# Optimization experiments

Measured on AMD Instinct MI355X. Metric: run time of the kernel, lower is better.

## Reference

```python
import jax, jax.numpy as jnp
import numpy as np

RHO = 0.5
MASK = 1.0
FR0 = 4096  # ifft length along fast-time axis
FR1 = 512   # fft length along slow-time (Doppler) axis
WIN = 8     # sliding-window length of the phase-reference accumulator
EPS_DENOM = 1e-6


def setup_inputs() -> dict:
    key = jax.random.key(0)
    k1, k2 = jax.random.split(key)
    x_real = jax.random.normal(k1, (8, 4096, 256), dtype=jnp.float32)
    x_imag = jax.random.normal(k2, (8, 4096, 256), dtype=jnp.float32)
    return {"x_real": x_real, "x_imag": x_imag}


def _phase_com_doppler(inp):
    # inp: [B, N, M_in] complex; ifft along last axis padded/truncated to FR0
    final = jnp.fft.ifft(inp, n=FR0, axis=2)  # [B, N, M]
    B, N, M = final.shape
    out0 = final[:, 0, :]                      # [B, M]
    # reproduces the torch `if k < 7` branch without control flow.
    buf0 = jnp.zeros((WIN, B, M), final.dtype).at[WIN - 1].set(out0)

    def step(carry, f_k1):
        pref, buf = carry
        s = jnp.sum(jnp.conj(pref) * f_k1, axis=-1, keepdims=True)  # [B,1]
        phase = s / jnp.abs(s)
        o = f_k1 * jnp.conj(phase)                                  # [B,M]
        pref = pref + o - buf[0]
        buf = jnp.concatenate([buf[1:], o[None]], axis=0)
        return (pref, buf), o

    seq = jnp.swapaxes(final, 0, 1)[1:]        # [N-1, B, M]
    _, outs = jax.lax.scan(step, (out0, buf0), seq)
    out = jnp.concatenate([out0[None], outs], axis=0)  # [N, B, M]
    out = jnp.swapaxes(out, 0, 1)              # [B, N, M]
    # fft along pulse axis padded to FR1
    return jnp.fft.fft(out, n=FR1, axis=1)     # [B, FR1, M]


def reference(x_real, x_imag):
    x = jax.lax.complex(x_real, x_imag)        # [B, P, Q] complex64
    denom = MASK + RHO
    denom = EPS_DENOM if denom == 0 else denom
    x2 = x * (1.0 / denom)
    out3 = _phase_com_doppler(jnp.swapaxes(x2, -1, -2))  # [B, FR1, FR0]
    out3 = jnp.swapaxes(out3, -1, -2)          # [B, FR0, FR1]
    # cs_data dict -> tuple ('input', 'nnline_input')
    return (x, out3)
```

## Files before the change

### kernel.cpp

```cpp
#include <hip/hip_runtime.h>
#include <math.h>

#define NF 4096
#define NC 256
#define NJ 512
#define CH 128
#define TWO_PI_F 6.28318530717958647692f

__device__ __forceinline__ float2 cmul(float2 a, float2 b) {
    return make_float2(a.x*b.x - a.y*b.y, a.x*b.y + a.y*b.x);
}

__device__ __forceinline__ void dft4i(float2& x0, float2& x1, float2& x2, float2& x3, float sgn) {
    float2 t0 = make_float2(x0.x + x2.x, x0.y + x2.y);
    float2 t1 = make_float2(x0.x - x2.x, x0.y - x2.y);
    float2 t2 = make_float2(x1.x + x3.x, x1.y + x3.y);
    float2 t3 = make_float2(x1.x - x3.x, x1.y - x3.y);
    float2 it3 = make_float2(-sgn * t3.y, sgn * t3.x);
    x0 = make_float2(t0.x + t2.x, t0.y + t2.y);
    x2 = make_float2(t0.x - t2.x, t0.y - t2.y);
    x1 = make_float2(t1.x + it3.x, t1.y + it3.y);
    x3 = make_float2(t1.x - it3.x, t1.y - it3.y);
}

__device__ __forceinline__ void dft16(float2* u, float sgn) {
    dft4i(u[0], u[4], u[8],  u[12], sgn);
    dft4i(u[1], u[5], u[9],  u[13], sgn);
    dft4i(u[2], u[6], u[10], u[14], sgn);
    dft4i(u[3], u[7], u[11], u[15], sgn);
    const float C1 = 0.9238795325112867f, S1 = 0.3826834323650898f, R2 = 0.7071067811865476f;
    u[5]  = cmul(u[5],  make_float2(C1,  sgn * S1));
    u[6]  = cmul(u[6],  make_float2(R2,  sgn * R2));
    u[7]  = cmul(u[7],  make_float2(S1,  sgn * C1));
    u[9]  = cmul(u[9],  make_float2(R2,  sgn * R2));
    u[10] = cmul(u[10], make_float2(0.f, sgn));
    u[11] = cmul(u[11], make_float2(-R2, sgn * R2));
    u[13] = cmul(u[13], make_float2(S1,  sgn * C1));
    u[14] = cmul(u[14], make_float2(-R2, sgn * R2));
    u[15] = cmul(u[15], make_float2(-C1, -sgn * S1));
    dft4i(u[0],  u[1],  u[2],  u[3],  sgn);
    dft4i(u[4],  u[5],  u[6],  u[7],  sgn);
    dft4i(u[8],  u[9],  u[10], u[11], sgn);
    dft4i(u[12], u[13], u[14], u[15], sgn);
}

__device__ __forceinline__ void dft8(const float2* u, float2* v, float sgn) {
    float2 e0 = u[0], e1 = u[2], e2 = u[4], e3 = u[6];
    float2 o0 = u[1], o1 = u[3], o2 = u[5], o3 = u[7];
    dft4i(e0, e1, e2, e3, sgn);
    dft4i(o0, o1, o2, o3, sgn);
    const float R2 = 0.7071067811865476f;
    float2 w1 = make_float2(R2, sgn * R2);
    float2 w2 = make_float2(0.f, sgn);
    float2 w3 = make_float2(-R2, sgn * R2);
    float2 t1 = cmul(o1, w1), t2 = cmul(o2, w2), t3 = cmul(o3, w3);
    v[0] = make_float2(e0.x + o0.x, e0.y + o0.y);
    v[4] = make_float2(e0.x - o0.x, e0.y - o0.y);
    v[1] = make_float2(e1.x + t1.x, e1.y + t1.y);
    v[5] = make_float2(e1.x - t1.x, e1.y - t1.y);
    v[2] = make_float2(e2.x + t2.x, e2.y + t2.y);
    v[6] = make_float2(e2.x - t2.x, e2.y - t2.y);
    v[3] = make_float2(e3.x + t3.x, e3.y + t3.y);
    v[7] = make_float2(e3.x - t3.x, e3.y - t3.y);
}

__global__ __launch_bounds__(256) void transpose_kernel(const float* __restrict__ xr,
                                                        const float* __restrict__ xi,
                                                        float2* __restrict__ fin,
                                                        int b0, int nbm1, int nbshift) {
    __shared__ float ldr[64][65];
    __shared__ float ldi[64][65];
    int wg = blockIdx.x;
    int bl = wg & nbm1;
    int rest = wg >> nbshift;
    int ft = rest & 63;
    int ct = rest >> 6;
    int f0 = ft << 6, c0 = ct << 6;
    int t = threadIdx.x;
    int cl = t & 63;
    int rq = t >> 6;
    const float scale = 1.0f / (4096.0f * 1.5f);
    int bg = b0 + bl;
    const float* xrb = xr + (size_t)bg * NF * NC;
    const float* xib = xi + (size_t)bg * NF * NC;
#pragma unroll
    for (int q = 0; q < 16; q++) {
        int r = q * 4 + rq;
        size_t idx = (size_t)(f0 + r) * NC + c0 + cl;
        ldr[cl][r] = xrb[idx] * scale;
        ldi[cl][r] = xib[idx] * scale;
    }
    __syncthreads();
    int fl = t & 63;
#pragma unroll
    for (int q = 0; q < 16; q++) {
        int cr = q * 4 + rq;
        fin[((size_t)(bl * NC + c0 + cr)) * NF + f0 + fl] =
            make_float2(ldr[cr][fl], ldi[cr][fl]);
    }
}

#define IPAD(a) ((a) + ((a) >> 4))

template<int P>
__device__ __forceinline__ void pass16(float2* S, int t, float sgn) {
    const int k = t & (P - 1);
    float2 u[16];
#pragma unroll
    for (int r = 0; r < 16; r++) u[r] = S[IPAD(t + 256 * r)];
    __syncthreads();
    if (P > 1) {
        float ab = sgn * (TWO_PI_F / (16.0f * (float)P)) * (float)k;
#pragma unroll
        for (int r = 1; r < 16; r++) {
            float sn, cs; __sincosf(ab * (float)r, &sn, &cs);
            u[r] = cmul(u[r], make_float2(cs, sn));
        }
    }
    dft16(u, sgn);
    const int base = 16 * P * (t / P) + k;
#pragma unroll
    for (int j = 0; j < 16; j++) {
        const int sl = ((j & 3) << 2) | (j >> 2);
        S[IPAD(base + j * P)] = u[sl];
    }
    __syncthreads();
}

__global__ __launch_bounds__(256) void ifft4096_kernel(float2* __restrict__ fin,
                                                       int bmask, int bshift) {
    __shared__ float2 S[4352];
    int wg = blockIdx.x;
    int bl = wg & bmask;
    int c = wg >> bshift;
    int t = threadIdx.x;
    size_t base = ((size_t)(bl * NC + c)) * NF;
    const float4* g4 = (const float4*)(fin + base);
#pragma unroll
    for (int q = 0; q < 8; q++) {
        float4 v = g4[t + 256 * q];
        int f = 2 * (t + 256 * q);
        S[IPAD(f)]     = make_float2(v.x, v.y);
        S[IPAD(f + 1)] = make_float2(v.z, v.w);
    }
    __syncthreads();
    pass16<1>(S, t, 1.0f);
    pass16<16>(S, t, 1.0f);
    pass16<256>(S, t, 1.0f);
    float4* o4 = (float4*)(fin + base);
#pragma unroll
    for (int q = 0; q < 8; q++) {
        int f = 2 * (t + 256 * q);
        float2 a = S[IPAD(f)];
        float2 b = S[IPAD(f + 1)];
        o4[t + 256 * q] = make_float4(a.x, a.y, b.x, b.y);
    }
}

#define GST 142
__global__ __launch_bounds__(256) void gram_kernel(const float2* __restrict__ fin,
                                                   float2* __restrict__ gpart) {
    __shared__ float2 lfc[40 * GST];
    int wg = blockIdx.x;
    int bl = wg >> 8;
    int ks = (wg >> 5) & 7;
    int ch = wg & 31;
    int m0 = ch * CH;
    int k0 = ks * 32;
    int t = threadIdx.x;
#pragma unroll
    for (int q = 0; q < 20; q++) {
        int e = t + 256 * q;
        int row = e >> 7;
        int m = e & 127;
        int gk = k0 - 8 + row;
        float2 v = (gk >= 0) ? fin[((size_t)(bl * NC + gk)) * NF + m0 + m]
                             : make_float2(0.f, 0.f);
        lfc[row * GST + 18 * (m >> 4) + (m & 15)] = v;
    }
    __syncthreads();
    int kk = t >> 4;
    int sg = t & 15;
    int sbase = 18 * (sg >> 1) + 8 * (sg & 1);
    double a0x[8], a0y[8], a1x[8], a1y[8];
#pragma unroll
    for (int d = 0; d < 8; d++) { a0x[d] = 0.0; a0y[d] = 0.0; a1x[d] = 0.0; a1y[d] = 0.0; }
    const float2* rbase = &lfc[2 * kk * GST + sbase];
#pragma unroll
    for (int mm = 0; mm < 8; mm += 2) {
        float4 r[10];
#pragma unroll
        for (int j = 0; j < 10; j++)
            r[j] = *(const float4*)(rbase + j * GST + mm);
        float4 b0 = r[8];
        float4 b1 = r[9];
#pragma unroll
        for (int d = 1; d <= 8; d++) {
            float4 aa = r[8 - d];
            a0x[d - 1] = fma((double)aa.y, (double)b0.y,
                         fma((double)aa.x, (double)b0.x, a0x[d - 1]));
            a0y[d - 1] = fma((double)aa.x, (double)b0.y,
                         fma(-(double)aa.y, (double)b0.x, a0y[d - 1]));
            a0x[d - 1] = fma((double)aa.w, (double)b0.w,
                         fma((double)aa.z, (double)b0.z, a0x[d - 1]));
            a0y[d - 1] = fma((double)aa.z, (double)b0.w,
                         fma(-(double)aa.w, (double)b0.z, a0y[d - 1]));
            float4 ab = r[9 - d];
            a1x[d - 1] = fma((double)ab.y, (double)b1.y,
                         fma((double)ab.x, (double)b1.x, a1x[d - 1]));
            a1y[d - 1] = fma((double)ab.x, (double)b1.y,
                         fma(-(double)ab.y, (double)b1.x, a1y[d - 1]));
            a1x[d - 1] = fma((double)ab.w, (double)b1.w,
                         fma((double)ab.z, (double)b1.z, a1x[d - 1]));
            a1y[d - 1] = fma((double)ab.z, (double)b1.w,
                         fma(-(double)ab.w, (double)b1.z, a1y[d - 1]));
        }
    }
    size_t gb0 = ((size_t)(bl * 32 + ch) * NC + (k0 + 2 * kk)) * 8;
#pragma unroll
    for (int d = 0; d < 8; d++) {
        double sx0 = a0x[d], sy0 = a0y[d], sx1 = a1x[d], sy1 = a1y[d];
#pragma unroll
        for (int off = 1; off <= 8; off <<= 1) {
            sx0 += __shfl_xor(sx0, off);
            sy0 += __shfl_xor(sy0, off);
            sx1 += __shfl_xor(sx1, off);
            sy1 += __shfl_xor(sy1, off);
        }
        if (sg == 0) {
            gpart[gb0 + d]     = make_float2((float)sx0, (float)sy0);
            gpart[gb0 + 8 + d] = make_float2((float)sx1, (float)sy1);
        }
    }
}

__global__ void gsum_kernel(const float2* __restrict__ gpart, float2* __restrict__ gs, int total) {
    int e = blockIdx.x * blockDim.x + threadIdx.x;
    if (e >= total) return;
    int bl = e >> 11;
    int kd = e & 2047;
    float2 s = make_float2(0.f, 0.f);
    for (int ch = 0; ch < 32; ch++) {
        float2 v = gpart[((size_t)(bl * 32 + ch)) * 2048 + kd];
        s.x += v.x; s.y += v.y;
    }
    gs[e] = s;
}

#define SCAN_STEP(A0, A1, A2, A3, KIDX)  do {                                  \
    float rx0 = p1.x*A0.x - p1.y*A0.y, ry0 = p1.x*A0.y + p1.y*A0.x;            \
    float rx1 = p2.x*A0.z - p2.y*A0.w, ry1 = p2.x*A0.w + p2.y*A0.z;            \
    float rx2 = p3.x*A1.x - p3.y*A1.y, ry2 = p3.x*A1.y + p3.y*A1.x;            \
    float rx3 = p4.x*A1.z - p4.y*A1.w, ry3 = p4.x*A1.w + p4.y*A1.z;            \
    float rx4 = p5.x*A2.x - p5.y*A2.y, ry4 = p5.x*A2.y + p5.y*A2.x;            \
    float rx5 = p6.x*A2.z - p6.y*A2.w, ry5 = p6.x*A2.w + p6.y*A2.z;            \
    float rx6 = p7.x*A3.x - p7.y*A3.y, ry6 = p7.x*A3.y + p7.y*A3.x;            \
    float rx7 = p8.x*A3.z - p8.y*A3.w, ry7 = p8.x*A3.w + p8.y*A3.z;            \
    float sx = ((rx0 + rx1) + (rx2 + rx3)) + ((rx4 + rx5) + (rx6 + rx7));      \
    float sy = ((ry0 + ry1) + (ry2 + ry3)) + ((ry4 + ry5) + (ry6 + ry7));      \
    float inv = rsqrtf(sx * sx + sy * sy);                                     \
    float2 np = make_float2(sx * inv, sy * inv);                               \
    phase[t * NC + (KIDX)] = np;                                               \
    p8 = p7; p7 = p6; p6 = p5; p5 = p4; p4 = p3; p3 = p2; p2 = p1; p1 = np;    \
} while (0)

#define SCAN_LOADG4(BUF, KBASE)  do {                                          \
    _Pragma("unroll") for (int j = 0; j < 4; j++) {                            \
        _Pragma("unroll") for (int q = 0; q < 4; q++)                          \
            BUF[j][q] = gb4[((KBASE) + j) * 4 + q];                            \
    }                                                                          \
} while (0)

#define SCAN_GRP4(BUF, KBASE, FIRST)  do {                                     \
    _Pragma("unroll") for (int j = 0; j < 4; j++) {                            \
        if (FIRST && j == 0) {                                                 \
            phase[t * NC] = make_float2(1.f, 0.f);                             \
        } else {                                                               \
            SCAN_STEP(BUF[j][0], BUF[j][1], BUF[j][2], BUF[j][3], (KBASE) + j);\
        }                                                                      \
    }                                                                          \
} while (0)

__global__ __launch_bounds__(64, 1) void scan_copy_kernel(const float2* __restrict__ gs,
                                                          float2* __restrict__ phase, int nb,
                                                          const float4* __restrict__ csrc,
                                                          float4* __restrict__ cdst, int cn4) {
    if (blockIdx.x != 0) {
        int i = (blockIdx.x - 1) * 64 + threadIdx.x;
        int stride = (gridDim.x - 1) * 64;
        for (; i < cn4; i += stride) cdst[i] = csrc[i];
        return;
    }
    int t = threadIdx.x;
    if (t >= nb) return;
    const float4* gb4 = (const float4*)(gs + (size_t)t * 2048);
    float2 z = make_float2(0.f, 0.f);
    float2 p1 = make_float2(1.f, 0.f);
    float2 p2 = z, p3 = z, p4 = z, p5 = z, p6 = z, p7 = z, p8 = z;
    float4 B0[4][4], B1[4][4], B2[4][4], B3[4][4];
    SCAN_LOADG4(B0, 0);
    SCAN_LOADG4(B1, 4);
    SCAN_LOADG4(B2, 8);
    __builtin_amdgcn_sched_barrier(0);
    for (int i = 0; i < 16; i++) {
        int k0 = i * 16;
        SCAN_LOADG4(B3, k0 + 12);
        __builtin_amdgcn_sched_barrier(0);
        if (i == 0) { SCAN_GRP4(B0, k0, true); } else { SCAN_GRP4(B0, k0, false); }
        SCAN_LOADG4(B0, k0 + 16);
        __builtin_amdgcn_sched_barrier(0);
        SCAN_GRP4(B1, k0 + 4, false);
        SCAN_LOADG4(B1, k0 + 20);
        __builtin_amdgcn_sched_barrier(0);
        SCAN_GRP4(B2, k0 + 8, false);
        SCAN_LOADG4(B2, k0 + 24);
        __builtin_amdgcn_sched_barrier(0);
        SCAN_GRP4(B3, k0 + 12, false);
    }
}

__global__ void scale_kernel(float4* __restrict__ fin4, const float2* __restrict__ phase, int n4) {
    int i = blockIdx.x * blockDim.x + threadIdx.x;
    if (i >= n4) return;
    int row = i >> 11;
    float2 ph = phase[row];
    float4 v = fin4[i];
    fin4[i] = make_float4(v.x*ph.x + v.y*ph.y, v.y*ph.x - v.x*ph.y,
                          v.z*ph.x + v.w*ph.y, v.w*ph.x - v.z*ph.y);
}

#define FPAD 516

template<int P, bool ZTOP>
__device__ __forceinline__ void pass8x(float2* L, int fp, int i2, float sgn) {
    const int ia = i2, ib = i2 + 32;
    const int ka = ia & (P - 1), kb = ib & (P - 1);
    float2 ua[8], ub[8];
#pragma unroll
    for (int r = 0; r < 8; r++) {
        if (ZTOP && r >= 4) {
            ua[r] = make_float2(0.f, 0.f);
            ub[r] = make_float2(0.f, 0.f);
        } else {
            ua[r] = L[fp * FPAD + ia + 64 * r];
            ub[r] = L[fp * FPAD + ib + 64 * r];
        }
    }
    __syncthreads();
    if (P > 1) {
        float aba = sgn * (TWO_PI_F / (8.0f * (float)P)) * (float)ka;
        float abb = sgn * (TWO_PI_F / (8.0f * (float)P)) * (float)kb;
#pragma unroll
        for (int r = 1; r < 8; r++) {
            float sn, cs;
            __sincosf(aba * (float)r, &sn, &cs);
            ua[r] = cmul(ua[r], make_float2(cs, sn));
            __sincosf(abb * (float)r, &sn, &cs);
            ub[r] = cmul(ub[r], make_float2(cs, sn));
        }
    }
    float2 va[8], vb[8];
    dft8(ua, va, sgn);
    dft8(ub, vb, sgn);
    const int basea = 8 * P * (ia / P) + ka;
    const int baseb = 8 * P * (ib / P) + kb;
#pragma unroll
    for (int r = 0; r < 8; r++) {
        L[fp * FPAD + basea + r * P] = va[r];
        L[fp * FPAD + baseb + r * P] = vb[r];
    }
    __syncthreads();
}

__global__ __launch_bounds__(256) void fft512_kernel(const float2* __restrict__ fin,
                                                     const float2* __restrict__ ph,
                                                     float* __restrict__ outr,
                                                     float2* __restrict__ outc,
                                                     int b0, int realOnly) {
    __shared__ float2 L[8 * FPAD];
    int wg = blockIdx.x;
    int bl = wg >> 9;
    int f0 = (wg & 511) * 8;
    int t = threadIdx.x;
    int fpp = t & 7;
    int cg = t >> 3;
#pragma unroll
    for (int it = 0; it < 8; it++) {
        int c = it * 32 + cg;
        float2 v = fin[((size_t)(bl * NC + c)) * NF + f0 + fpp];
        if (ph) {
            float2 p = ph[bl * NC + c];
            v = make_float2(v.x * p.x + v.y * p.y, v.y * p.x - v.x * p.y);
        }
        L[fpp * FPAD + c] = v;
    }
    __syncthreads();
    int fp = t & 7;
    int i2 = t >> 3;
    pass8x<1, true >(L, fp, i2, -1.0f);
    pass8x<8, false>(L, fp, i2, -1.0f);
    pass8x<64, false>(L, fp, i2, -1.0f);
    size_t ob = ((size_t)((b0 + bl) * NF + f0)) * NJ;
    if (realOnly) {
#pragma unroll
        for (int fp2 = 0; fp2 < 8; fp2++) {
            int j = 2 * t;
            float2 w = make_float2(L[fp2 * FPAD + j].x, L[fp2 * FPAD + j + 1].x);
            *(float2*)&outr[ob + (size_t)fp2 * NJ + j] = w;
        }
    } else {
#pragma unroll
        for (int fp2 = 0; fp2 < 8; fp2++)
#pragma unroll
            for (int jq = 0; jq < 2; jq++) {
                int j = t + 256 * jq;
                outc[ob + (size_t)fp2 * NJ + j] = L[fp2 * FPAD + j];
            }
    }
}

__global__ void copy_kernel(const float4* __restrict__ src, float4* __restrict__ dst, int n4) {
    int i = blockIdx.x * blockDim.x + threadIdx.x;
    int stride = gridDim.x * blockDim.x;
    for (; i < n4; i += stride) dst[i] = src[i];
}
__global__ void pack_x_kernel(const float2* __restrict__ xr, const float2* __restrict__ xi,
                              float4* __restrict__ out, int n4) {
    int i = blockIdx.x * blockDim.x + threadIdx.x;
    int stride = gridDim.x * blockDim.x;
    for (; i < n4; i += stride) {
        float2 r = xr[i], m = xi[i];
        out[i] = make_float4(r.x, m.x, r.y, m.y);
    }
}

extern "C" void kernel_launch(void* const* d_in, const int* in_sizes, int n_in,
                              void* d_out, int out_size, void* d_ws, size_t ws_size,
                              hipStream_t stream) {
    const float* xr = (const float*)d_in[0];
    const float* xi = (const float*)d_in[1];
    float* out = (float*)d_out;

    if (out_size < 40000000) {
        float* out0r = out;
        float* out3r = out + 8388608;
        size_t need = (size_t)(8388608 + 524288 + 16384 + 2048) * sizeof(float2);
        if (ws_size >= need) {
            float2* fin   = (float2*)d_ws;
            float2* gpart = fin + 8388608;
            float2* gsb   = gpart + 524288;
            float2* phase = gsb + 16384;
            transpose_kernel<<<8 * 256, 256, 0, stream>>>(xr, xi, fin, 0, 7, 3);
            ifft4096_kernel<<<8 * NC, 256, 0, stream>>>(fin, 7, 3);
            gram_kernel<<<8 * 256, 256, 0, stream>>>(fin, gpart);
            gsum_kernel<<<(8 * 2048) / 256, 256, 0, stream>>>(gpart, gsb, 8 * 2048);
            scan_copy_kernel<<<2049, 64, 0, stream>>>(gsb, phase, 8,
                                                      (const float4*)xr, (float4*)out0r, 2097152);
            fft512_kernel<<<8 * 512, 256, 0, stream>>>(fin, phase, out3r, nullptr, 0, 1);
        } else {
            float2* fin   = (float2*)out0r;
            float2* o3f2  = (float2*)out3r;
            float2* gpart = o3f2 + (8388608 - 262144 - 8192 - 1024);
            float2* gsb   = o3f2 + (8388608 - 8192 - 1024);
            float2* phase = o3f2 + (8388608 - 1024);
            for (int p = 0; p < 2; p++) {
                int b0 = p * 4;
                transpose_kernel<<<4 * 256, 256, 0, stream>>>(xr, xi, fin, b0, 3, 2);
                ifft4096_kernel<<<4 * NC, 256, 0, stream>>>(fin, 3, 2);
                gram_kernel<<<4 * 256, 256, 0, stream>>>(fin, gpart);
                gsum_kernel<<<(4 * 2048) / 256, 256, 0, stream>>>(gpart, gsb, 4 * 2048);
                scan_copy_kernel<<<1, 64, 0, stream>>>(gsb, phase, 4, nullptr, nullptr, 0);
                scale_kernel<<<4 * 2048, 256, 0, stream>>>((float4*)fin, phase, 4 * 524288);
                fft512_kernel<<<4 * 512, 256, 0, stream>>>(fin, nullptr, out3r, nullptr, b0, 1);
            }
            copy_kernel<<<2048, 256, 0, stream>>>((const float4*)xr, (float4*)out0r, 2097152);
        }
    } else {
        float2* out0f2 = (float2*)out;
        float2* out3f2 = (float2*)(out + 16777216);
        float2* fin   = out0f2;
        float2* gpart = out3f2 + (16777216 - 524288 - 16384 - 2048);
        float2* gsb   = out3f2 + (16777216 - 16384 - 2048);
        float2* phase = out3f2 + (16777216 - 2048);
        transpose_kernel<<<8 * 256, 256, 0, stream>>>(xr, xi, fin, 0, 7, 3);
        ifft4096_kernel<<<8 * NC, 256, 0, stream>>>(fin, 7, 3);
        gram_kernel<<<8 * 256, 256, 0, stream>>>(fin, gpart);
        gsum_kernel<<<(8 * 2048) / 256, 256, 0, stream>>>(gpart, gsb, 8 * 2048);
        scan_copy_kernel<<<1, 64, 0, stream>>>(gsb, phase, 8, nullptr, nullptr, 0);
        scale_kernel<<<8 * 2048, 256, 0, stream>>>((float4*)fin, phase, 8 * 524288);
        fft512_kernel<<<8 * 512, 256, 0, stream>>>(fin, nullptr, nullptr, out3f2, 0, 0);
        pack_x_kernel<<<4096, 256, 0, stream>>>((const float2*)xr, (const float2*)xi,
                                                (float4*)out0f2, 4194304);
    }
}
```

Baseline: 169.3 us.

## Compute lag Gram from raw input via Parseval and fuse kernels

```diff
diff --git a/kernel.cpp b/kernel.cpp
--- a/kernel.cpp
+++ b/kernel.cpp
@@ -64,13 +64,9 @@
     v[7] = make_float2(e3.x - t3.x, e3.y - t3.y);
 }
 
-__global__ __launch_bounds__(256) void transpose_kernel(const float* __restrict__ xr,
-                                                        const float* __restrict__ xi,
-                                                        float2* __restrict__ fin,
-                                                        int b0, int nbm1, int nbshift) {
-    __shared__ float ldr[64][65];
-    __shared__ float ldi[64][65];
-    int wg = blockIdx.x;
+__device__ __forceinline__ void transpose_body(float* ldr, float* ldi,
+                                               const float* xr, const float* xi,
+                                               float2* fin, int wg, int b0, int nbm1, int nbshift) {
     int bl = wg & nbm1;
     int rest = wg >> nbshift;
     int ft = rest & 63;
@@ -87,8 +83,8 @@
     for (int q = 0; q < 16; q++) {
         int r = q * 4 + rq;
         size_t idx = (size_t)(f0 + r) * NC + c0 + cl;
-        ldr[cl][r] = xrb[idx] * scale;
-        ldi[cl][r] = xib[idx] * scale;
+        ldr[cl * 65 + r] = xrb[idx] * scale;
+        ldi[cl * 65 + r] = xib[idx] * scale;
     }
     __syncthreads();
     int fl = t & 63;
@@ -96,7 +92,7 @@
     for (int q = 0; q < 16; q++) {
         int cr = q * 4 + rq;
         fin[((size_t)(bl * NC + c0 + cr)) * NF + f0 + fl] =
-            make_float2(ldr[cr][fl], ldi[cr][fl]);
+            make_float2(ldr[cr * 65 + fl], ldi[cr * 65 + fl]);
     }
 }
 
@@ -127,10 +123,7 @@
     __syncthreads();
 }
 
-__global__ __launch_bounds__(256) void ifft4096_kernel(float2* __restrict__ fin,
-                                                       int bmask, int bshift) {
-    __shared__ float2 S[4352];
-    int wg = blockIdx.x;
+__device__ __forceinline__ void ifft_body(float2* S, float2* fin, int wg, int bmask, int bshift) {
     int bl = wg & bmask;
     int c = wg >> bshift;
     int t = threadIdx.x;
@@ -157,7 +150,133 @@
     }
 }
 
+__global__ __launch_bounds__(256) void transpose_kernel(const float* __restrict__ xr,
+                                                        const float* __restrict__ xi,
+                                                        float2* __restrict__ fin,
+                                                        int b0, int nbm1, int nbshift) {
+    __shared__ float ld[2 * 64 * 65];
+    transpose_body(ld, ld + 64 * 65, xr, xi, fin, blockIdx.x, b0, nbm1, nbshift);
+}
+
+__global__ __launch_bounds__(256) void ifft4096_kernel(float2* __restrict__ fin,
+                                                       int bmask, int bshift) {
+    __shared__ float2 S[4352];
+    ifft_body(S, fin, blockIdx.x, bmask, bshift);
+}
+
 #define GST 142
+__device__ __forceinline__ void gramx_body(float2* lfc, const float* xr, const float* xi,
+                                           float2* gpart, int wg) {
+    int bl = wg >> 8;
+    int cb = (wg >> 5) & 7;
+    int fc = wg & 31;
+    int c0 = cb * 32;
+    int F0 = fc * 128;
+    int t = threadIdx.x;
+#pragma unroll
+    for (int q = 0; q < 20; q++) {
+        int e = t + 256 * q;
+        int f_l = e / 40;
+        int c_l = e - 40 * f_l;
+        int gc = c0 - 8 + c_l;
+        float2 v = make_float2(0.f, 0.f);
+        if (gc >= 0) {
+            size_t idx = ((size_t)(bl * NF + F0 + f_l)) * NC + gc;
+            v = make_float2(xr[idx], xi[idx]);
+        }
+        lfc[c_l * GST + 18 * (f_l >> 4) + (f_l & 15)] = v;
+    }
+    __syncthreads();
+    int kk = t >> 4;
+    int sg = t & 15;
+    int sbase = 18 * (sg >> 1) + 8 * (sg & 1);
+    double a0x[8], a0y[8], a1x[8], a1y[8];
+#pragma unroll
+    for (int d = 0; d < 8; d++) { a0x[d] = 0.0; a0y[d] = 0.0; a1x[d] = 0.0; a1y[d] = 0.0; }
+    const float2* rbase = &lfc[2 * kk * GST + sbase];
+#pragma unroll
+    for (int mm = 0; mm < 8; mm += 2) {
+        float4 r[10];
+#pragma unroll
+        for (int j = 0; j < 10; j++)
+            r[j] = *(const float4*)(rbase + j * GST + mm);
+        float4 b0 = r[8];
+        float4 b1 = r[9];
+#pragma unroll
+        for (int d = 1; d <= 8; d++) {
+            float4 aa = r[8 - d];
+            a0x[d - 1] = fma((double)aa.y, (double)b0.y,
+                         fma((double)aa.x, (double)b0.x, a0x[d - 1]));
+            a0y[d - 1] = fma((double)aa.x, (double)b0.y,
+                         fma(-(double)aa.y, (double)b0.x, a0y[d - 1]));
+            a0x[d - 1] = fma((double)aa.w, (double)b0.w,
+                         fma((double)aa.z, (double)b0.z, a0x[d - 1]));
+            a0y[d - 1] = fma((double)aa.z, (double)b0.w,
+                         fma(-(double)aa.w, (double)b0.z, a0y[d - 1]));
+            float4 ab = r[9 - d];
+            a1x[d - 1] = fma((double)ab.y, (double)b1.y,
+                         fma((double)ab.x, (double)b1.x, a1x[d - 1]));
+            a1y[d - 1] = fma((double)ab.x, (double)b1.y,
+                         fma(-(double)ab.y, (double)b1.x, a1y[d - 1]));
+            a1x[d - 1] = fma((double)ab.w, (double)b1.w,
+                         fma((double)ab.z, (double)b1.z, a1x[d - 1]));
+            a1y[d - 1] = fma((double)ab.z, (double)b1.w,
+                         fma(-(double)ab.w, (double)b1.z, a1y[d - 1]));
+        }
+    }
+    const double SCL = 1.0 / (4096.0 * 2.25);
+    size_t gb0 = ((size_t)(bl * 32 + fc) * NC + (c0 + 2 * kk)) * 8;
+#pragma unroll
+    for (int d = 0; d < 8; d++) {
+        double sx0 = a0x[d], sy0 = a0y[d], sx1 = a1x[d], sy1 = a1y[d];
+#pragma unroll
+        for (int off = 1; off <= 8; off <<= 1) {
+            sx0 += __shfl_xor(sx0, off);
+            sy0 += __shfl_xor(sy0, off);
+            sx1 += __shfl_xor(sx1, off);
+            sy1 += __shfl_xor(sy1, off);
+        }
+        if (sg == 0) {
+            gpart[gb0 + d]     = make_float2((float)(sx0 * SCL), (float)(sy0 * SCL));
+            gpart[gb0 + 8 + d] = make_float2((float)(sx1 * SCL), (float)(sy1 * SCL));
+        }
+    }
+}
+
+__global__ __launch_bounds__(256) void k1_transpose_gramx(const float* __restrict__ xr,
+                                                          const float* __restrict__ xi,
+                                                          float2* __restrict__ fin,
+                                                          float2* __restrict__ gpart) {
+    __shared__ float2 lfc[40 * GST];
+    if (blockIdx.x < 2048) {
+        float* ldr = (float*)lfc;
+        transpose_body(ldr, ldr + 64 * 65, xr, xi, fin, blockIdx.x, 0, 7, 3);
+    } else {
+        gramx_body(lfc, xr, xi, gpart, blockIdx.x - 2048);
+    }
+}
+
+__global__ __launch_bounds__(256) void k2_ifft_gsum(float2* __restrict__ fin,
+                                                    const float2* __restrict__ gpart,
+                                                    float2* __restrict__ gs) {
+    __shared__ float2 S[4352];
+    if (blockIdx.x < 2048) {
+        ifft_body(S, fin, blockIdx.x, 7, 3);
+    } else {
+        int e = (blockIdx.x - 2048) * 256 + threadIdx.x;
+        if (e < 16384) {
+            int bl = e >> 11;
+            int kd = e & 2047;
+            float2 s = make_float2(0.f, 0.f);
+            for (int ch = 0; ch < 32; ch++) {
+                float2 v = gpart[((size_t)(bl * 32 + ch)) * 2048 + kd];
+                s.x += v.x; s.y += v.y;
+            }
+            gs[e] = s;
+        }
+    }
+}
+
 __global__ __launch_bounds__(256) void gram_kernel(const float2* __restrict__ fin,
                                                    float2* __restrict__ gpart) {
     __shared__ float2 lfc[40 * GST];
@@ -450,10 +569,8 @@
             float2* gpart = fin + 8388608;
             float2* gsb   = gpart + 524288;
             float2* phase = gsb + 16384;
-            transpose_kernel<<<8 * 256, 256, 0, stream>>>(xr, xi, fin, 0, 7, 3);
-            ifft4096_kernel<<<8 * NC, 256, 0, stream>>>(fin, 7, 3);
-            gram_kernel<<<8 * 256, 256, 0, stream>>>(fin, gpart);
-            gsum_kernel<<<(8 * 2048) / 256, 256, 0, stream>>>(gpart, gsb, 8 * 2048);
+            k1_transpose_gramx<<<4096, 256, 0, stream>>>(xr, xi, fin, gpart);
+            k2_ifft_gsum<<<2112, 256, 0, stream>>>(fin, gpart, gsb);
             scan_copy_kernel<<<2049, 64, 0, stream>>>(gsb, phase, 8,
                                                       (const float4*)xr, (float4*)out0r, 2097152);
             fft512_kernel<<<8 * 512, 256, 0, stream>>>(fin, phase, out3r, nullptr, 0, 1);
```

After: 180.1 us. +6.3%, slower.

## Move output copy into gram kernel and widen transpose memory accesses

Applied to the files above, without the earlier changes.

```diff
diff --git a/kernel.cpp b/kernel.cpp
--- a/kernel.cpp
+++ b/kernel.cpp
@@ -77,26 +77,31 @@
     int ct = rest >> 6;
     int f0 = ft << 6, c0 = ct << 6;
     int t = threadIdx.x;
-    int cl = t & 63;
-    int rq = t >> 6;
     const float scale = 1.0f / (4096.0f * 1.5f);
     int bg = b0 + bl;
     const float* xrb = xr + (size_t)bg * NF * NC;
     const float* xib = xi + (size_t)bg * NF * NC;
-#pragma unroll
-    for (int q = 0; q < 16; q++) {
-        int r = q * 4 + rq;
-        size_t idx = (size_t)(f0 + r) * NC + c0 + cl;
-        ldr[cl][r] = xrb[idx] * scale;
-        ldi[cl][r] = xib[idx] * scale;
-    }
-    __syncthreads();
-    int fl = t & 63;
-#pragma unroll
-    for (int q = 0; q < 16; q++) {
-        int cr = q * 4 + rq;
-        fin[((size_t)(bl * NC + c0 + cr)) * NF + f0 + fl] =
-            make_float2(ldr[cr][fl], ldi[cr][fl]);
+    int cl2 = t & 31;
+    int rq = t >> 5;
+#pragma unroll
+    for (int q = 0; q < 8; q++) {
+        int r = q * 8 + rq;
+        size_t idx = (size_t)(f0 + r) * NC + c0 + 2 * cl2;
+        float2 vr = *(const float2*)&xrb[idx];
+        float2 vi = *(const float2*)&xib[idx];
+        ldr[2 * cl2][r]     = vr.x * scale;
+        ldr[2 * cl2 + 1][r] = vr.y * scale;
+        ldi[2 * cl2][r]     = vi.x * scale;
+        ldi[2 * cl2 + 1][r] = vi.y * scale;
+    }
+    __syncthreads();
+    int fl2 = t & 31;
+#pragma unroll
+    for (int q = 0; q < 8; q++) {
+        int cr = q * 8 + rq;
+        float4 w = make_float4(ldr[cr][2 * fl2],     ldi[cr][2 * fl2],
+                               ldr[cr][2 * fl2 + 1], ldi[cr][2 * fl2 + 1]);
+        *(float4*)&fin[((size_t)(bl * NC + c0 + cr)) * NF + f0 + 2 * fl2] = w;
     }
 }
 
@@ -158,10 +163,18 @@
 }
 
 #define GST 142
-__global__ __launch_bounds__(256) void gram_kernel(const float2* __restrict__ fin,
-                                                   float2* __restrict__ gpart) {
+__global__ __launch_bounds__(256) void gram_copy_kernel(const float2* __restrict__ fin,
+                                                        float2* __restrict__ gpart,
+                                                        const float4* __restrict__ csrc,
+                                                        float4* __restrict__ cdst, int cn4) {
     __shared__ float2 lfc[40 * GST];
     int wg = blockIdx.x;
+    if (wg >= 2048) {
+        int i = (wg - 2048) * 256 + threadIdx.x;
+        int stride = 2048 * 256;
+        for (; i < cn4; i += stride) cdst[i] = csrc[i];
+        return;
+    }
     int bl = wg >> 8;
     int ks = (wg >> 5) & 7;
     int ch = wg & 31;
@@ -281,16 +294,8 @@
     }                                                                          \
 } while (0)
 
-__global__ __launch_bounds__(64, 1) void scan_copy_kernel(const float2* __restrict__ gs,
-                                                          float2* __restrict__ phase, int nb,
-                                                          const float4* __restrict__ csrc,
-                                                          float4* __restrict__ cdst, int cn4) {
-    if (blockIdx.x != 0) {
-        int i = (blockIdx.x - 1) * 64 + threadIdx.x;
-        int stride = (gridDim.x - 1) * 64;
-        for (; i < cn4; i += stride) cdst[i] = csrc[i];
-        return;
-    }
+__global__ __launch_bounds__(64, 1) void scan_kernel(const float2* __restrict__ gs,
+                                                     float2* __restrict__ phase, int nb) {
     int t = threadIdx.x;
     if (t >= nb) return;
     const float4* gb4 = (const float4*)(gs + (size_t)t * 2048);
@@ -452,10 +457,10 @@
             float2* phase = gsb + 16384;
             transpose_kernel<<<8 * 256, 256, 0, stream>>>(xr, xi, fin, 0, 7, 3);
             ifft4096_kernel<<<8 * NC, 256, 0, stream>>>(fin, 7, 3);
-            gram_kernel<<<8 * 256, 256, 0, stream>>>(fin, gpart);
+            gram_copy_kernel<<<4096, 256, 0, stream>>>(fin, gpart,
+                                                       (const float4*)xr, (float4*)out0r, 2097152);
             gsum_kernel<<<(8 * 2048) / 256, 256, 0, stream>>>(gpart, gsb, 8 * 2048);
-            scan_copy_kernel<<<2049, 64, 0, stream>>>(gsb, phase, 8,
-                                                      (const float4*)xr, (float4*)out0r, 2097152);
+            scan_kernel<<<1, 64, 0, stream>>>(gsb, phase, 8);
             fft512_kernel<<<8 * 512, 256, 0, stream>>>(fin, phase, out3r, nullptr, 0, 1);
         } else {
             float2* fin   = (float2*)out0r;
@@ -467,9 +472,9 @@
                 int b0 = p * 4;
                 transpose_kernel<<<4 * 256, 256, 0, stream>>>(xr, xi, fin, b0, 3, 2);
                 ifft4096_kernel<<<4 * NC, 256, 0, stream>>>(fin, 3, 2);
-                gram_kernel<<<4 * 256, 256, 0, stream>>>(fin, gpart);
+                gram_copy_kernel<<<4 * 256, 256, 0, stream>>>(fin, gpart, nullptr, nullptr, 0);
                 gsum_kernel<<<(4 * 2048) / 256, 256, 0, stream>>>(gpart, gsb, 4 * 2048);
-                scan_copy_kernel<<<1, 64, 0, stream>>>(gsb, phase, 4, nullptr, nullptr, 0);
+                scan_kernel<<<1, 64, 0, stream>>>(gsb, phase, 4);
                 scale_kernel<<<4 * 2048, 256, 0, stream>>>((float4*)fin, phase, 4 * 524288);
                 fft512_kernel<<<4 * 512, 256, 0, stream>>>(fin, nullptr, out3r, nullptr, b0, 1);
             }
@@ -484,9 +489,9 @@
         float2* phase = out3f2 + (16777216 - 2048);
         transpose_kernel<<<8 * 256, 256, 0, stream>>>(xr, xi, fin, 0, 7, 3);
         ifft4096_kernel<<<8 * NC, 256, 0, stream>>>(fin, 7, 3);
-        gram_kernel<<<8 * 256, 256, 0, stream>>>(fin, gpart);
+        gram_copy_kernel<<<8 * 256, 256, 0, stream>>>(fin, gpart, nullptr, nullptr, 0);
         gsum_kernel<<<(8 * 2048) / 256, 256, 0, stream>>>(gpart, gsb, 8 * 2048);
-        scan_copy_kernel<<<1, 64, 0, stream>>>(gsb, phase, 8, nullptr, nullptr, 0);
+        scan_kernel<<<1, 64, 0, stream>>>(gsb, phase, 8);
         scale_kernel<<<8 * 2048, 256, 0, stream>>>((float4*)fin, phase, 8 * 524288);
         fft512_kernel<<<8 * 512, 256, 0, stream>>>(fin, nullptr, nullptr, out3f2, 0, 0);
         pack_x_kernel<<<4096, 256, 0, stream>>>((const float2*)xr, (const float2*)xi,
```

New measurement: 175.7 us. +3.8%, slower.
